# Kernel tuning notes

Measured on AMD Instinct MI355X. Metric: run time of the kernel, lower is better.

The kernel has to match this reference:

```python
import jax, jax.numpy as jnp
import numpy as np

N = 100000   # nodes
E = 400000   # edges (avg degree 4, NoC-mesh-like)
H = 512      # hidden_channels
F_IN = 1     # num_node_features


def _lin(key, fan_in, fan_out):
    # torch.nn.Linear default init: U(-1/sqrt(fan_in), 1/sqrt(fan_in))
    bound = 1.0 / np.sqrt(fan_in)
    return jax.random.uniform(key, (fan_in, fan_out), jnp.float32, -bound, bound)


def setup_inputs() -> dict:
    key = jax.random.key(0)
    ks = jax.random.split(key, 16)
    inp = {
        "x": jax.random.normal(ks[0], (N, F_IN), jnp.float32),
        "edge_index": jax.random.randint(ks[1], (2, E), 0, N, jnp.int32),
        # conv1: in=1 -> out=512
        "w_rel1": _lin(ks[2], F_IN, H),
        "b_rel1": jax.random.uniform(ks[3], (H,), jnp.float32, -1.0, 1.0),
        "w_root1": _lin(ks[4], F_IN, H),
        # conv2..4: 512 -> 512
        "w_rel2": _lin(ks[5], H, H),
        "b_rel2": jax.random.uniform(ks[6], (H,), jnp.float32, -1/np.sqrt(H), 1/np.sqrt(H)),
        "w_root2": _lin(ks[7], H, H),
        "w_rel3": _lin(ks[8], H, H),
        "b_rel3": jax.random.uniform(ks[9], (H,), jnp.float32, -1/np.sqrt(H), 1/np.sqrt(H)),
        "w_root3": _lin(ks[10], H, H),
        "w_rel4": _lin(ks[11], H, H),
        "b_rel4": jax.random.uniform(ks[12], (H,), jnp.float32, -1/np.sqrt(H), 1/np.sqrt(H)),
        "w_root4": _lin(ks[13], H, H),
    }
    return inp


def _graph_conv(x, src, dst, w_rel, b_rel, w_root):
    # PyG GraphConv (aggr='add'): out_i = W_rel @ sum_{j in N(i)} x_j + b_rel + W_root @ x_i
    # messages flow src (edge_index[0]) -> dst (edge_index[1])
    agg = jax.ops.segment_sum(x[src], dst, num_segments=N)  # [N, F_in]
    return agg @ w_rel + b_rel + x @ w_root


def reference(x, edge_index,
              w_rel1, b_rel1, w_root1,
              w_rel2, b_rel2, w_root2,
              w_rel3, b_rel3, w_root3,
              w_rel4, b_rel4, w_root4):
    src, dst = edge_index[0], edge_index[1]
    x1 = jax.nn.relu(_graph_conv(x,  src, dst, w_rel1, b_rel1, w_root1))
    x2 = jax.nn.relu(_graph_conv(x1, src, dst, w_rel2, b_rel2, w_root2)) + x1
    x3 = _graph_conv(x2, src, dst, w_rel3, b_rel3, w_root3) + x2
    x4 = _graph_conv(x3, src, dst, w_rel4, b_rel4, w_root4) + x3
    return x4
```

## Files before the change

kernel.cpp:

```cpp
#include <hip/hip_runtime.h>

#define NN 100000
#define EE 400000
#define HH 512
#define NB_SCAN 98

typedef __attribute__((ext_vector_type(8))) short short8;
typedef __attribute__((ext_vector_type(8))) unsigned short ushort8;
typedef __attribute__((ext_vector_type(4))) float f32x4;

__device__ inline unsigned short f2b(float f) {
    unsigned int u = __float_as_uint(f);
    return (unsigned short)((u + 0x7fffu + ((u >> 16) & 1u)) >> 16);
}
__device__ inline float b2f(unsigned short b) {
    return __uint_as_float(((unsigned int)b) << 16);
}

__global__ void histo_deg(const int* __restrict__ dst, int* __restrict__ deg) {
    int e = blockIdx.x * blockDim.x + threadIdx.x;
    if (e < EE) atomicAdd(&deg[dst[e]], 1);
}

__global__ void scan_reduce(const int* __restrict__ deg, int* __restrict__ blockSums) {
    __shared__ int s[256];
    int b = blockIdx.x, t = threadIdx.x;
    int base = b * 1024 + t * 4;
    int v = 0;
    #pragma unroll
    for (int j = 0; j < 4; ++j) { int i = base + j; if (i < NN) v += deg[i]; }
    s[t] = v; __syncthreads();
    for (int off = 128; off > 0; off >>= 1) {
        if (t < off) s[t] += s[t + off];
        __syncthreads();
    }
    if (t == 0) blockSums[b] = s[0];
}

__global__ void scan_top(int* __restrict__ blockSums, int* __restrict__ start) {
    __shared__ int s[128];
    int t = threadIdx.x;
    s[t] = (t < NB_SCAN) ? blockSums[t] : 0;
    __syncthreads();
    for (int off = 1; off < 128; off <<= 1) {
        int u = (t >= off) ? s[t - off] : 0;
        __syncthreads();
        s[t] += u;
        __syncthreads();
    }
    if (t < NB_SCAN) blockSums[t] = (t == 0) ? 0 : s[t - 1];
    if (t == 0) start[NN] = EE;
}

__global__ void scan_down(const int* __restrict__ deg, const int* __restrict__ blockSums,
                          int* __restrict__ start, int* __restrict__ cursor) {
    __shared__ int s[256];
    int b = blockIdx.x, t = threadIdx.x;
    int base = b * 1024 + t * 4;
    int v[4]; int sum = 0;
    #pragma unroll
    for (int j = 0; j < 4; ++j) {
        int i = base + j;
        v[j] = (i < NN) ? deg[i] : 0;
        sum += v[j];
    }
    s[t] = sum; __syncthreads();
    for (int off = 1; off < 256; off <<= 1) {
        int u = (t >= off) ? s[t - off] : 0;
        __syncthreads();
        s[t] += u;
        __syncthreads();
    }
    int excl = blockSums[b] + ((t == 0) ? 0 : s[t - 1]);
    #pragma unroll
    for (int j = 0; j < 4; ++j) {
        int i = base + j;
        if (i < NN) { start[i] = excl; cursor[i] = excl; excl += v[j]; }
    }
}

__global__ void csr_fill(const int* __restrict__ src, const int* __restrict__ dst,
                         int* __restrict__ cursor, int* __restrict__ eidx) {
    int e = blockIdx.x * blockDim.x + threadIdx.x;
    if (e < EE) {
        int p = atomicAdd(&cursor[dst[e]], 1);
        eidx[p] = src[e];
    }
}

__global__ void w_transpose_all(
    const float* __restrict__ w0, const float* __restrict__ w1,
    const float* __restrict__ w2, const float* __restrict__ w3,
    const float* __restrict__ w4, const float* __restrict__ w5,
    unsigned short* __restrict__ wt)
{
    int m = blockIdx.x >> 10;
    int idx = ((blockIdx.x & 1023) << 8) + threadIdx.x;
    int n = idx >> 9, k = idx & 511;
    const float* w = (m == 0) ? w0 : (m == 1) ? w1 : (m == 2) ? w2
                   : (m == 3) ? w3 : (m == 4) ? w4 : w5;
    size_t pos = ((size_t)(n >> 7) << 16) + (((k >> 5) & 15) << 12) + ((n & 127) << 5)
               + (((((k >> 3) & 3) ^ ((n >> 1) & 3))) << 3) + (k & 7);
    wt[(size_t)m * 262144 + pos] = f2b(w[(size_t)k * HH + n]);
}

__global__ __launch_bounds__(256) void gather_rows_b(
    const unsigned short* __restrict__ xb, const int* __restrict__ start,
    const int* __restrict__ eidx, unsigned short* __restrict__ agg)
{
    int node = blockIdx.x * 4 + (threadIdx.x >> 6);
    if (node >= NN) return;
    int l = threadIdx.x & 63;
    int c0 = l << 3;
    float a[8] = {0.f,0.f,0.f,0.f,0.f,0.f,0.f,0.f};
    int e0 = start[node], e1 = start[node + 1];
    int e = e0;
    for (; e + 4 <= e1; e += 4) {
        int s0 = eidx[e], s1 = eidx[e + 1], s2 = eidx[e + 2], s3 = eidx[e + 3];
        ushort8 v0 = *(const ushort8*)(xb + (size_t)s0 * HH + c0);
        ushort8 v1 = *(const ushort8*)(xb + (size_t)s1 * HH + c0);
        ushort8 v2 = *(const ushort8*)(xb + (size_t)s2 * HH + c0);
        ushort8 v3 = *(const ushort8*)(xb + (size_t)s3 * HH + c0);
        #pragma unroll
        for (int j = 0; j < 8; ++j)
            a[j] += (b2f(v0[j]) + b2f(v1[j])) + (b2f(v2[j]) + b2f(v3[j]));
    }
    for (; e < e1; ++e) {
        ushort8 v = *(const ushort8*)(xb + (size_t)eidx[e] * HH + c0);
        #pragma unroll
        for (int j = 0; j < 8; ++j) a[j] += b2f(v[j]);
    }
    ushort8 o;
    #pragma unroll
    for (int j = 0; j < 8; ++j) o[j] = f2b(a[j]);
    size_t pa = ((size_t)(node >> 7) << 16) + ((size_t)(l >> 2) << 12)
              + ((size_t)(node & 127) << 5)
              + ((size_t)(((l & 3) ^ ((node >> 1) & 3)) << 3));
    *(ushort8*)(agg + pa) = o;
}

__global__ void gather_scalar(const float* __restrict__ x, const int* __restrict__ start,
                              const int* __restrict__ eidx, float* __restrict__ agg0) {
    int i = blockIdx.x * blockDim.x + threadIdx.x;
    if (i >= NN) return;
    float s = 0.f;
    int e1 = start[i + 1];
    for (int e = start[i]; e < e1; ++e) s += x[eidx[e]];
    agg0[i] = s;
}

__global__ void layer1_expand(const float* __restrict__ x,
                              const float* __restrict__ agg0,
                              const float* __restrict__ w_rel,
                              const float* __restrict__ b,
                              const float* __restrict__ w_root,
                              unsigned short* __restrict__ x1b) {
    int idx = blockIdx.x * blockDim.x + threadIdx.x;
    int i = idx >> 7;
    if (i >= NN) return;
    int q = (idx & 127) << 2;
    float a = agg0[i], xv = x[i];
    float4 wr = *(const float4*)&w_rel[q];
    float4 bb = *(const float4*)&b[q];
    float4 wt = *(const float4*)&w_root[q];
    float4 o;
    o.x = fmaxf(fmaf(a, wr.x, fmaf(xv, wt.x, bb.x)), 0.f);
    o.y = fmaxf(fmaf(a, wr.y, fmaf(xv, wt.y, bb.y)), 0.f);
    o.z = fmaxf(fmaf(a, wr.z, fmaf(xv, wt.z, bb.z)), 0.f);
    o.w = fmaxf(fmaf(a, wr.w, fmaf(xv, wt.w, bb.w)), 0.f);
    ushort4 ob = { f2b(o.x), f2b(o.y), f2b(o.z), f2b(o.w) };
    *(ushort4*)&x1b[(size_t)i * HH + q] = ob;
}

__device__ inline void gload16(const void* g, void* l) {
    __builtin_amdgcn_global_load_lds(
        (const __attribute__((address_space(1))) unsigned int*)g,
        (__attribute__((address_space(3))) unsigned int*)l,
        16, 0, 0);
}

template<bool RELU, bool F32OUT>
__global__ __launch_bounds__(256, 3) void gemm_mfma(
    const unsigned short* __restrict__ AB, const unsigned short* __restrict__ XBp,
    const unsigned short* __restrict__ WrT, const unsigned short* __restrict__ WoT,
    const float* __restrict__ bias, const unsigned short* __restrict__ residb,
    float* __restrict__ out, unsigned short* __restrict__ outb)
{
    __shared__ unsigned short As[2 * 128 * 32];
    __shared__ unsigned short Bs[2 * 128 * 32];
    const int tid  = threadIdx.x;
    const int wave = tid >> 6, lane = tid & 63;

    const int bid = blockIdx.x;
    const int nid = (bid & 7) * 391 + (bid >> 3);
    const int col0 = (nid & 3) << 7;
    const int row0 = (nid >> 2) << 7;
    const int rb = nid >> 2;
    const int cb = nid & 3;

    const int wr = wave >> 1, wc = wave & 1;
    const int l16 = lane & 15, lq = lane >> 4;
    const int sRow = lane >> 2;
    const int sColSwz = (((lane & 3) ^ ((lane >> 3) & 3)) << 3);
    const int xorslot = ((lq ^ ((lane >> 1) & 3)) << 3);

    int rowA[2];
    #pragma unroll
    for (int i = 0; i < 2; ++i) {
        int chunk = (wave << 1) + i;
        int gr = row0 + chunk * 16 + sRow;
        rowA[i] = (gr >= NN) ? (NN - 1) : gr;
    }

    f32x4 acc[4][4];
    #pragma unroll
    for (int m = 0; m < 4; ++m)
        #pragma unroll
        for (int n = 0; n < 4; ++n) acc[m][n] = (f32x4){0.f,0.f,0.f,0.f};

    auto STAGE = [&](unsigned short* Asb, unsigned short* Bsb, int t) {
        const int c = t & 15;
        {
            const unsigned short* Wp = (t < 16) ? WrT : WoT;
            const unsigned short* srcB = Wp + ((size_t)cb << 16) + (c << 12);
            #pragma unroll
            for (int i = 0; i < 2; ++i) {
                int j = (wave << 1) + i;
                gload16(srcB + (j << 9) + (lane << 3), Bsb + (j << 9));
            }
        }
        if (t < 16) {
            const unsigned short* srcA = AB + ((size_t)rb << 16) + (c << 12);
            #pragma unroll
            for (int i = 0; i < 2; ++i) {
                int j = (wave << 1) + i;
                gload16(srcA + (j << 9) + (lane << 3), Asb + (j << 9));
            }
        } else {
            const int kk = c << 5;
            #pragma unroll
            for (int i = 0; i < 2; ++i) {
                int chunk = (wave << 1) + i;
                gload16(XBp + (size_t)rowA[i] * HH + kk + sColSwz, Asb + chunk * 512);
            }
        }
    };
    auto COMPUTE = [&](const unsigned short* Asb, const unsigned short* Bsb) {
        short8 af[4], bfv[4];
        #pragma unroll
        for (int m = 0; m < 4; ++m)
            af[m] = *(const short8*)(Asb + (wr * 64 + m * 16 + l16) * 32 + xorslot);
        #pragma unroll
        for (int n = 0; n < 4; ++n)
            bfv[n] = *(const short8*)(Bsb + (wc * 64 + n * 16 + l16) * 32 + xorslot);
        #pragma unroll
        for (int m = 0; m < 4; ++m)
            #pragma unroll
            for (int n = 0; n < 4; ++n)
                acc[m][n] = __builtin_amdgcn_mfma_f32_16x16x32_bf16(af[m], bfv[n], acc[m][n], 0, 0, 0);
    };

    unsigned short *A0 = As, *A1 = As + 4096, *B0 = Bs, *B1 = Bs + 4096;
    STAGE(A0, B0, 0);
    __syncthreads();
    #pragma unroll 1
    for (int t = 0; t < 32; t += 2) {
        STAGE(A1, B1, t + 1);
        COMPUTE(A0, B0);
        __syncthreads();
        if (t + 2 < 32) STAGE(A0, B0, t + 2);
        COMPUTE(A1, B1);
        __syncthreads();
    }

    float bias_n[4];
    #pragma unroll
    for (int n = 0; n < 4; ++n) bias_n[n] = bias[col0 + wc * 64 + n * 16 + l16];

    #pragma unroll
    for (int m = 0; m < 4; ++m) {
        #pragma unroll
        for (int j = 0; j < 4; ++j) {
            int row = row0 + wr * 64 + m * 16 + lq * 4 + j;
            if (row >= NN) continue;
            #pragma unroll
            for (int n = 0; n < 4; ++n) {
                int col = col0 + wc * 64 + n * 16 + l16;
                size_t off = (size_t)row * HH + col;
                float v = acc[m][n][j] + bias_n[n];
                if (RELU) v = fmaxf(v, 0.f);
                v += b2f(residb[off]);
                if (F32OUT) out[off] = v;
                else        outb[off] = f2b(v);
            }
        }
    }
}

extern "C" void kernel_launch(void* const* d_in, const int* in_sizes, int n_in,
                              void* d_out, int out_size, void* d_ws, size_t ws_size,
                              hipStream_t stream) {
    const float* x   = (const float*)d_in[0];
    const int*   ei  = (const int*)d_in[1];
    const int*   src = ei;
    const int*   dst = ei + EE;
    const float* w_rel1  = (const float*)d_in[2];
    const float* b_rel1  = (const float*)d_in[3];
    const float* w_root1 = (const float*)d_in[4];
    const float* w_rel2  = (const float*)d_in[5];
    const float* b_rel2  = (const float*)d_in[6];
    const float* w_root2 = (const float*)d_in[7];
    const float* w_rel3  = (const float*)d_in[8];
    const float* b_rel3  = (const float*)d_in[9];
    const float* w_root3 = (const float*)d_in[10];
    const float* w_rel4  = (const float*)d_in[11];
    const float* b_rel4  = (const float*)d_in[12];
    const float* w_root4 = (const float*)d_in[13];

    const size_t NH  = (size_t)NN * HH;
    const size_t NHP = (size_t)100096 * HH;
    unsigned short* XB   = (unsigned short*)d_ws;
    unsigned short* XB2  = XB + NH;
    unsigned short* X3B  = XB2 + NH;
    unsigned short* AGB  = X3B + NH;
    unsigned short* WT   = AGB + NHP;
    float*          agg0 = (float*)(WT + 6 * 262144);
    int*            csr  = (int*)(agg0 + NN);
    int* deg       = csr;
    int* start     = csr + NN;
    int* cursor    = start + NN + 1;
    int* eidx      = cursor + NN;
    int* blockSums = eidx + EE;
    float* out = (float*)d_out;

    unsigned short* WrT2 = WT;
    unsigned short* WoT2 = WT + 1 * 262144;
    unsigned short* WrT3 = WT + 2 * 262144;
    unsigned short* WoT3 = WT + 3 * 262144;
    unsigned short* WrT4 = WT + 4 * 262144;
    unsigned short* WoT4 = WT + 5 * 262144;

    const int gGemm = 3128;

    hipMemsetAsync(deg, 0, NN * sizeof(int), stream);
    histo_deg<<<(EE + 255) / 256, 256, 0, stream>>>(dst, deg);
    scan_reduce<<<NB_SCAN, 256, 0, stream>>>(deg, blockSums);
    scan_top<<<1, 128, 0, stream>>>(blockSums, start);
    scan_down<<<NB_SCAN, 256, 0, stream>>>(deg, blockSums, start, cursor);
    csr_fill<<<(EE + 255) / 256, 256, 0, stream>>>(src, dst, cursor, eidx);

    w_transpose_all<<<6144, 256, 0, stream>>>(
        w_rel2, w_root2, w_rel3, w_root3, w_rel4, w_root4, WT);

    gather_scalar<<<(NN + 255) / 256, 256, 0, stream>>>(x, start, eidx, agg0);
    layer1_expand<<<50000, 256, 0, stream>>>(x, agg0, w_rel1, b_rel1, w_root1, XB);

    gather_rows_b<<<25000, 256, 0, stream>>>(XB, start, eidx, AGB);
    gemm_mfma<true, false><<<gGemm, 256, 0, stream>>>(
        AGB, XB, WrT2, WoT2, b_rel2, XB, nullptr, XB2);

    gather_rows_b<<<25000, 256, 0, stream>>>(XB2, start, eidx, AGB);
    gemm_mfma<false, false><<<gGemm, 256, 0, stream>>>(
        AGB, XB2, WrT3, WoT3, b_rel3, XB2, nullptr, X3B);

    gather_rows_b<<<25000, 256, 0, stream>>>(X3B, start, eidx, AGB);
    gemm_mfma<false, true><<<gGemm, 256, 0, stream>>>(
        AGB, X3B, WrT4, WoT4, b_rel4, X3B, out, nullptr);
}
```

Measured before the change: 762.3 us.

## Replace 4-wave block GEMM with single-wave 64x64 tiles and triple-buffered loads

The fused GEMM now runs as one 64-thread wave per 64x64 output tile instead of a 256-thread block per 128x128 tile, with four times as many blocks. Staging uses three LDS buffers with manual s_waitcnt vmcnt counters instead of __syncthreads, so loads for two stages ahead overlap the MFMA compute without any barriers. The cost is less reuse per tile: each weight and activation chunk is loaded from global memory twice as often. The code also assumes the pre-tiled AGB/weight layouts can be indexed at 64-row granularity.

```diff
diff --git a/kernel.cpp b/kernel.cpp
--- a/kernel.cpp
+++ b/kernel.cpp
@@ -180,35 +180,34 @@
 }
 
 template<bool RELU, bool F32OUT>
-__global__ __launch_bounds__(256, 3) void gemm_mfma(
+__global__ __launch_bounds__(64) void gemm_wave(
     const unsigned short* __restrict__ AB, const unsigned short* __restrict__ XBp,
     const unsigned short* __restrict__ WrT, const unsigned short* __restrict__ WoT,
     const float* __restrict__ bias, const unsigned short* __restrict__ residb,
     float* __restrict__ out, unsigned short* __restrict__ outb)
 {
-    __shared__ unsigned short As[2 * 128 * 32];
-    __shared__ unsigned short Bs[2 * 128 * 32];
-    const int tid  = threadIdx.x;
-    const int wave = tid >> 6, lane = tid & 63;
+    __shared__ unsigned short As[3 * 2048];
+    __shared__ unsigned short Bs[3 * 2048];
+    const int lane = threadIdx.x;
 
     const int bid = blockIdx.x;
-    const int nid = (bid & 7) * 391 + (bid >> 3);
-    const int col0 = (nid & 3) << 7;
-    const int row0 = (nid >> 2) << 7;
-    const int rb = nid >> 2;
-    const int cb = nid & 3;
-
-    const int wr = wave >> 1, wc = wave & 1;
+    const int nid = (bid & 7) * 1563 + (bid >> 3);
+    const int ntile = nid & 7;
+    const int mtile = nid >> 3;
+    const int col0 = ntile << 6;
+    const int row0 = mtile << 6;
+
     const int l16 = lane & 15, lq = lane >> 4;
-    const int sRow = lane >> 2;
     const int sColSwz = (((lane & 3) ^ ((lane >> 3) & 3)) << 3);
     const int xorslot = ((lq ^ ((lane >> 1) & 3)) << 3);
 
-    int rowA[2];
-    #pragma unroll
-    for (int i = 0; i < 2; ++i) {
-        int chunk = (wave << 1) + i;
-        int gr = row0 + chunk * 16 + sRow;
+    const unsigned short* pA = AB + ((size_t)(mtile >> 1) << 16) + ((mtile & 1) << 11);
+    const size_t pBoff = ((size_t)(ntile >> 1) << 16) + ((ntile & 1) << 11);
+
+    int rowA[4];
+    #pragma unroll
+    for (int i = 0; i < 4; ++i) {
+        int gr = row0 + i * 16 + (lane >> 2);
         rowA[i] = (gr >= NN) ? (NN - 1) : gr;
     }
 
@@ -220,39 +219,30 @@
 
     auto STAGE = [&](unsigned short* Asb, unsigned short* Bsb, int t) {
         const int c = t & 15;
-        {
-            const unsigned short* Wp = (t < 16) ? WrT : WoT;
-            const unsigned short* srcB = Wp + ((size_t)cb << 16) + (c << 12);
+        const unsigned short* srcB = ((t < 16) ? WrT : WoT) + pBoff + (c << 12);
+        #pragma unroll
+        for (int i = 0; i < 4; ++i)
+            gload16(srcB + (i << 9) + (lane << 3), Bsb + (i << 9));
+        if (t < 16) {
+            const unsigned short* srcA = pA + (c << 12);
             #pragma unroll
-            for (int i = 0; i < 2; ++i) {
-                int j = (wave << 1) + i;
-                gload16(srcB + (j << 9) + (lane << 3), Bsb + (j << 9));
-            }
-        }
-        if (t < 16) {
-            const unsigned short* srcA = AB + ((size_t)rb << 16) + (c << 12);
-            #pragma unroll
-            for (int i = 0; i < 2; ++i) {
-                int j = (wave << 1) + i;
-                gload16(srcA + (j << 9) + (lane << 3), Asb + (j << 9));
-            }
+            for (int i = 0; i < 4; ++i)
+                gload16(srcA + (i << 9) + (lane << 3), Asb + (i << 9));
         } else {
             const int kk = c << 5;
             #pragma unroll
-            for (int i = 0; i < 2; ++i) {
-                int chunk = (wave << 1) + i;
-                gload16(XBp + (size_t)rowA[i] * HH + kk + sColSwz, Asb + chunk * 512);
-            }
+            for (int i = 0; i < 4; ++i)
+                gload16(XBp + (size_t)rowA[i] * HH + kk + sColSwz, Asb + (i << 9));
         }
     };
     auto COMPUTE = [&](const unsigned short* Asb, const unsigned short* Bsb) {
         short8 af[4], bfv[4];
         #pragma unroll
         for (int m = 0; m < 4; ++m)
-            af[m] = *(const short8*)(Asb + (wr * 64 + m * 16 + l16) * 32 + xorslot);
+            af[m] = *(const short8*)(Asb + (m * 16 + l16) * 32 + xorslot);
         #pragma unroll
         for (int n = 0; n < 4; ++n)
-            bfv[n] = *(const short8*)(Bsb + (wc * 64 + n * 16 + l16) * 32 + xorslot);
+            bfv[n] = *(const short8*)(Bsb + (n * 16 + l16) * 32 + xorslot);
         #pragma unroll
         for (int m = 0; m < 4; ++m)
             #pragma unroll
@@ -260,32 +250,42 @@
                 acc[m][n] = __builtin_amdgcn_mfma_f32_16x16x32_bf16(af[m], bfv[n], acc[m][n], 0, 0, 0);
     };
 
-    unsigned short *A0 = As, *A1 = As + 4096, *B0 = Bs, *B1 = Bs + 4096;
+    unsigned short *A0 = As, *A1 = As + 2048, *A2 = As + 4096;
+    unsigned short *B0 = Bs, *B1 = Bs + 2048, *B2 = Bs + 4096;
+
     STAGE(A0, B0, 0);
-    __syncthreads();
+    STAGE(A1, B1, 1);
+
     #pragma unroll 1
-    for (int t = 0; t < 32; t += 2) {
-        STAGE(A1, B1, t + 1);
+    for (int t = 0; t < 30; t += 3) {
+        asm volatile("s_waitcnt vmcnt(8)" ::: "memory");
+        STAGE(A2, B2, t + 2);
         COMPUTE(A0, B0);
-        __syncthreads();
-        if (t + 2 < 32) STAGE(A0, B0, t + 2);
+        asm volatile("s_waitcnt vmcnt(8)" ::: "memory");
+        STAGE(A0, B0, t + 3);
         COMPUTE(A1, B1);
-        __syncthreads();
-    }
+        asm volatile("s_waitcnt vmcnt(8)" ::: "memory");
+        if (t + 4 < 32) STAGE(A1, B1, t + 4);
+        COMPUTE(A2, B2);
+    }
+    asm volatile("s_waitcnt vmcnt(8)" ::: "memory");
+    COMPUTE(A0, B0);
+    asm volatile("s_waitcnt vmcnt(0)" ::: "memory");
+    COMPUTE(A1, B1);
 
     float bias_n[4];
     #pragma unroll
-    for (int n = 0; n < 4; ++n) bias_n[n] = bias[col0 + wc * 64 + n * 16 + l16];
+    for (int n = 0; n < 4; ++n) bias_n[n] = bias[col0 + n * 16 + l16];
 
     #pragma unroll
     for (int m = 0; m < 4; ++m) {
         #pragma unroll
         for (int j = 0; j < 4; ++j) {
-            int row = row0 + wr * 64 + m * 16 + lq * 4 + j;
+            int row = row0 + m * 16 + lq * 4 + j;
             if (row >= NN) continue;
             #pragma unroll
             for (int n = 0; n < 4; ++n) {
-                int col = col0 + wc * 64 + n * 16 + l16;
+                int col = col0 + n * 16 + l16;
                 size_t off = (size_t)row * HH + col;
                 float v = acc[m][n][j] + bias_n[n];
                 if (RELU) v = fmaxf(v, 0.f);
@@ -340,7 +340,7 @@
     unsigned short* WrT4 = WT + 4 * 262144;
     unsigned short* WoT4 = WT + 5 * 262144;
 
-    const int gGemm = 3128;
+    const int gGemm = 12504;
 
     hipMemsetAsync(deg, 0, NN * sizeof(int), stream);
     histo_deg<<<(EE + 255) / 256, 256, 0, stream>>>(dst, deg);
@@ -356,14 +356,14 @@
     layer1_expand<<<50000, 256, 0, stream>>>(x, agg0, w_rel1, b_rel1, w_root1, XB);
 
     gather_rows_b<<<25000, 256, 0, stream>>>(XB, start, eidx, AGB);
-    gemm_mfma<true, false><<<gGemm, 256, 0, stream>>>(
+    gemm_wave<true, false><<<gGemm, 64, 0, stream>>>(
         AGB, XB, WrT2, WoT2, b_rel2, XB, nullptr, XB2);
 
     gather_rows_b<<<25000, 256, 0, stream>>>(XB2, start, eidx, AGB);
-    gemm_mfma<false, false><<<gGemm, 256, 0, stream>>>(
+    gemm_wave<false, false><<<gGemm, 64, 0, stream>>>(
         AGB, XB2, WrT3, WoT3, b_rel3, XB2, nullptr, X3B);
 
     gather_rows_b<<<25000, 256, 0, stream>>>(X3B, start, eidx, AGB);
-    gemm_mfma<false, true><<<gGemm, 256, 0, stream>>>(
+    gemm_wave<false, true><<<gGemm, 64, 0, stream>>>(
         AGB, X3B, WrT4, WoT4, b_rel4, X3B, out, nullptr);
 }
```

After: 936.3 us. 22.8% more time.
